# Optimization experiments

Measured on AMD Instinct MI355X. Metric: run time of the kernel, lower is better.

## Reference

```python
import jax, jax.numpy as jnp
import numpy as np
from jax import lax

NP = 27  # num_param, perfect cube
N3 = 3   # cube root
EPS = 1e-5


def _conv3d(x, w, stride, pad):
    return lax.conv_general_dilated(
        x, w, window_strides=(stride,) * 3, padding=[(pad, pad)] * 3,
        dimension_numbers=("NCDHW", "OIDHW", "NCDHW"))


def _p_n():
    # torch.meshgrid(arange(3),arange(3),arange(3), indexing='xy') == np.meshgrid 'xy'
    g0, g1, g2 = np.meshgrid(np.arange(N3), np.arange(N3), np.arange(N3), indexing="xy")
    p_n = np.concatenate([g0.ravel(), g1.ravel(), g2.ravel()], 0)  # (3N,)
    return jnp.asarray(p_n, jnp.float32).reshape(1, 3 * NP, 1, 1, 1)


def _p_0(h, w, d):
    # faithful to original: 'xy' meshgrid, flatten, then view(1,1,h,w,d)
    g0, g1, g2 = np.meshgrid(np.arange(h), np.arange(w), np.arange(d), indexing="xy")
    outs = []
    for g in (g0, g1, g2):
        gg = jnp.asarray(g.ravel(), jnp.float32).reshape(1, 1, h, w, d)
        outs.append(jnp.broadcast_to(gg, (1, NP, h, w, d)))
    return jnp.concatenate(outs, axis=1)  # (1, 3N, h, w, d)


def _gather_xq(x_flat, ix, iy, iz, W, D, shape):
    # x_flat: (b, c, H*W*D); i*: (b, h, w, d, N) int32
    idx = ix * (W * D) + iy * D + iz
    b = idx.shape[0]
    idx = jnp.clip(idx, 0, x_flat.shape[-1] - 1).reshape(b, -1)
    xq = jax.vmap(lambda xf, ii: xf[:, ii])(x_flat, idx)  # (b, c, h*w*d*N)
    return xq.reshape(shape)


def reference(x, p_w, p_b, conv_w, gamma, beta):
    b, c, H, W, D = x.shape
    # offset prediction (weight is zero-initialized in original; bias drives offsets)
    offset = _conv3d(x, p_w, 1, 1) + p_b[None, :, None, None, None]  # (b, 3N, h, w, d)
    h, w, d = offset.shape[2:]

    p = _p_0(h, w, d) + _p_n() + offset                 # (b, 3N, h, w, d)
    p = jnp.transpose(p, (0, 2, 3, 4, 1))               # (b, h, w, d, 3N)
    px, py, pz = p[..., :NP], p[..., NP:2 * NP], p[..., 2 * NP:]

    fx, fy, fz = jnp.floor(px), jnp.floor(py), jnp.floor(pz)
    ltx = jnp.clip(fx, 0, H - 1); lty = jnp.clip(fy, 0, W - 1); ltz = jnp.clip(fz, 0, D - 1)
    rbx = jnp.clip(fx + 1, 0, H - 1); rby = jnp.clip(fy + 1, 0, W - 1); rbz = jnp.clip(fz + 1, 0, D - 1)

    pcx = jnp.clip(px, 0, H - 1); pcy = jnp.clip(py, 0, W - 1); pcz = jnp.clip(pz, 0, D - 1)

    # trilinear-style weights (6 corners as in the original)
    g_lt = (1 + (ltx - pcx)) * (1 + (lty - pcy)) * (1 + (ltz - pcz))
    g_rb = (1 - (rbx - pcx)) * (1 - (rby - pcy)) * (1 - (rbz - pcz))
    g_lb = (1 + (ltx - pcx)) * (1 - (rby - pcy)) * (1 + (ltz - pcz))
    g_rt = (1 - (rbx - pcx)) * (1 + (lty - pcy)) * (1 + (ltz - pcz))
    g_lf = (1 + (ltx - pcx)) * (1 + (lty - pcy)) * (1 - (rbz - pcz))
    g_rf = (1 - (rbx - pcx)) * (1 - (rby - pcy)) * (1 + (ltz - pcz))

    i = lambda t: t.astype(jnp.int32)
    x_flat = x.reshape(b, c, -1)
    shp = (b, c, h, w, d, NP)
    xq_lt = _gather_xq(x_flat, i(ltx), i(lty), i(ltz), W, D, shp)
    xq_rb = _gather_xq(x_flat, i(rbx), i(rby), i(rbz), W, D, shp)
    xq_lb = _gather_xq(x_flat, i(ltx), i(rby), i(ltz), W, D, shp)
    xq_rt = _gather_xq(x_flat, i(rbx), i(lty), i(ltz), W, D, shp)
    xq_lf = _gather_xq(x_flat, i(ltx), i(lty), i(rbz), W, D, shp)
    xq_rf = _gather_xq(x_flat, i(rbx), i(rby), i(ltz), W, D, shp)

    e = lambda g: g[:, None]  # (b,1,h,w,d,N)
    x_off = (e(g_lt) * xq_lt + e(g_rb) * xq_rb + e(g_lb) * xq_lb +
             e(g_rt) * xq_rt + e(g_lf) * xq_lf + e(g_rf) * xq_rf)

    # regroup (b,c,h,w,d,27) -> (b,c,3h,3w,3d)
    x_off = x_off.reshape(b, c, h, w, d, N3, N3, N3)
    x_off = jnp.transpose(x_off, (0, 1, 2, 5, 3, 6, 4, 7)).reshape(b, c, h * N3, w * N3, d * N3)

    # Conv3d(stride 2, pad 1, no bias) + BatchNorm3d (train mode, batch stats) + SiLU
    o = _conv3d(x_off, conv_w, 2, 1)
    mean = jnp.mean(o, axis=(0, 2, 3, 4), keepdims=True)
    var = jnp.var(o, axis=(0, 2, 3, 4), keepdims=True)
    y = gamma[None, :, None, None, None] * (o - mean) * lax.rsqrt(var + EPS) + beta[None, :, None, None, None]
    return y * jax.nn.sigmoid(y)


def setup_inputs() -> dict:
    key = jax.random.key(0)
    k1, k2, k3 = jax.random.split(key, 3)
    B, Cin, Cout, S = 2, 16, 32, 32
    x = jax.random.normal(k1, (B, Cin, S, S, S), jnp.float32)
    p_w = jnp.zeros((3 * NP, Cin, 3, 3, 3), jnp.float32)  # zero-init as in original
    bound = 1.0 / np.sqrt(Cin * 27)
    p_b = jax.random.uniform(k2, (3 * NP,), jnp.float32, -bound, bound)
    conv_w = jax.random.normal(k3, (Cout, Cin, 3, 3, 3), jnp.float32) * 0.05
    gamma = jnp.ones((Cout,), jnp.float32)
    beta = jnp.zeros((Cout,), jnp.float32)
    return {"x": x, "p_w": p_w, "p_b": p_b, "conv_w": conv_w, "gamma": gamma, "beta": beta}
```

## Files before the change

kernel.cpp:

```cpp
#include <hip/hip_runtime.h>
#include <hip/hip_bf16.h>

constexpr int BATCH = 2;
constexpr int CIN   = 16;
constexpr int COUT  = 32;
constexpr int HWD   = 32768;
constexpr int OFFC  = 81;
constexpr int BIG   = 96;
constexpr int BIG2  = BIG * BIG;
constexpr int BIGN  = BIG * BIG * BIG;
constexpr int OUTD  = 48;
constexpr int OUT2  = OUTD * OUTD;
constexpr int OUTN  = OUTD * OUTD * OUTD;
constexpr int NOUT  = BATCH * COUT * OUTN;
constexpr int NBLK3 = 1728;

typedef __attribute__((ext_vector_type(8)))  short bf16x8;
typedef __attribute__((ext_vector_type(16))) float f32x16;

__device__ __forceinline__ float bf_lo(uint u) { return __uint_as_float(u << 16); }
__device__ __forceinline__ float bf_hi(uint u) { return __uint_as_float(u & 0xFFFF0000u); }

__global__ __launch_bounds__(256) void k_wtrans(const float* __restrict__ cw,
                                                const float* __restrict__ pw,
                                                ushort* __restrict__ wTb,
                                                ushort* __restrict__ pwTb) {
    int t = blockIdx.x * 256 + threadIdx.x;
    if (t < 13824) {
        int ci = t & 15; int rr = t >> 4; int co = rr & 31; int tap = rr >> 5;
        float v = cw[co * 432 + ci * 27 + tap];
        __hip_bfloat16 h = __float2bfloat16(v);
        wTb[t] = *(ushort*)&h;
    } else if (t < 13824 + 41472) {
        int u = t - 13824;
        int ci = u & 15; int rr = u >> 4; int oc = rr % 96; int tap = rr / 96;
        float v = (oc < 81) ? pw[oc * 432 + ci * 27 + tap] : 0.f;
        __hip_bfloat16 h = __float2bfloat16(v);
        pwTb[u] = *(ushort*)&h;
    }
}

__global__ __launch_bounds__(256) void k_xt(const float* __restrict__ x,
                                            ushort* __restrict__ xb) {
    int t = blockIdx.x * 256 + threadIdx.x;
    int bt = t >> 15, pos = t & 32767;
    float v[16];
#pragma unroll
    for (int ci = 0; ci < 16; ci++) v[ci] = x[(bt * 16 + ci) * HWD + pos];
    uint uw[8];
#pragma unroll
    for (int cc = 0; cc < 8; cc++) {
        __hip_bfloat16 h0 = __float2bfloat16(v[2 * cc]);
        __hip_bfloat16 h1 = __float2bfloat16(v[2 * cc + 1]);
        uw[cc] = (uint)(*(ushort*)&h0) | ((uint)(*(ushort*)&h1) << 16);
    }
    uint4* xd = (uint4*)(xb + (size_t)t * 16);
    xd[0] = make_uint4(uw[0], uw[1], uw[2], uw[3]);
    xd[1] = make_uint4(uw[4], uw[5], uw[6], uw[7]);
}

__global__ __launch_bounds__(256) void k_offset_mfma(const ushort* __restrict__ xb,
                                                     const ushort* __restrict__ pwTb,
                                                     const float* __restrict__ p_b,
                                                     float* __restrict__ off) {
    __shared__ uint4 lds[4 * 10 * 11 * 2];
    int blk = blockIdx.x;
    int bt = blk >> 8; int r = blk & 255;
    int ut = r >> 4; int vt = (r >> 2) & 3; int wt = r & 3;
    int a0 = ut * 2, b0 = vt * 8, c0 = wt * 8;
    int tid = threadIdx.x;
    int wv = tid >> 6, l = tid & 63, col = l & 31, half = l >> 5;

    const ushort* xbb = xb + (size_t)bt * HWD * 16;
    for (int s = tid; s < 800; s += 256) {
        int h = s & 1, p = s >> 1;
        int su = p / 100; int rm = p - su * 100;
        int sv = rm / 10; int sw = rm - sv * 10;
        int ga = a0 - 1 + su, gb = b0 - 1 + sv, gc = c0 - 1 + sw;
        uint4 v = make_uint4(0, 0, 0, 0);
        if ((unsigned)ga < 32u && (unsigned)gb < 32u && (unsigned)gc < 32u)
            v = *(const uint4*)(xbb + (size_t)(ga * 1024 + gb * 32 + gc) * 16 + h * 8);
        lds[((su * 10 + sv) * 11 + sw) * 2 + h] = v;
    }
    __syncthreads();

    int U = wv >> 1, V = ((wv & 1) << 2) + (col >> 3), W = col & 7;
    const uint4* wt4 = (const uint4*)pwTb;
    int a = a0 + U, b = b0 + V, c = c0 + W;
    int pos = a * 1024 + b * 32 + c;
    float* ob = off + (size_t)bt * OFFC * HWD + pos;

#pragma unroll 1
    for (int g = 0; g < 3; g++) {
        bf16x8 wf[27];
#pragma unroll
        for (int t = 0; t < 27; t++)
            wf[t] = __builtin_bit_cast(bf16x8, wt4[(t * 96 + g * 32 + col) * 2 + half]);
        f32x16 acc;
#pragma unroll
        for (int i = 0; i < 16; i++) acc[i] = 0.f;
#pragma unroll
        for (int k1 = 0; k1 < 3; k1++)
#pragma unroll
        for (int k2 = 0; k2 < 3; k2++)
#pragma unroll
        for (int k3 = 0; k3 < 3; k3++) {
            bf16x8 xf = __builtin_bit_cast(bf16x8,
                lds[(((U + k1) * 10 + (V + k2)) * 11 + (W + k3)) * 2 + half]);
            acc = __builtin_amdgcn_mfma_f32_32x32x16_bf16(wf[(k1 * 3 + k2) * 3 + k3],
                                                          xf, acc, 0, 0, 0);
        }
#pragma unroll
        for (int rg = 0; rg < 16; rg++) {
            int co = g * 32 + (rg & 3) + 8 * (rg >> 2) + 4 * half;
            if (co < 81) ob[(size_t)co * HWD] = acc[rg] + p_b[co];
        }
    }
}

__global__ __launch_bounds__(256, 3) void k_fused(const ushort* __restrict__ xb,
                                                  const float* __restrict__ off,
                                                  const ushort* __restrict__ wTb,
                                                  ushort* __restrict__ o16,
                                                  float* __restrict__ psum,
                                                  float* __restrict__ psq) {
    __shared__ uint4 lds[5 * 17 * 19 * 2];
    __shared__ float ls[4][32], lq[4][32];

    int blk = blockIdx.x;
    int bt = blk / 864; int r = blk - bt * 864;
    int ut = r / 36; r -= ut * 36;
    int vt = r / 6;  int wt = r - vt * 6;

    int tid = threadIdx.x;
    int wv = tid >> 6, l = tid & 63;
    int col = l & 31, half = l >> 5;

    const ushort* xbb = xb + (size_t)bt * HWD * 16;
    const float* offb = off + (size_t)bt * OFFC * HWD;
    int gU0 = ut * 4 - 1, gV0 = vt * 16 - 1, gW0 = wt * 16 - 1;

    for (int s = tid; s < 1445; s += 256) {
        int su = s / 289; int rm = s - su * 289;
        int sv = rm / 17; int sw = rm - sv * 17;
        int gU = gU0 + su, gV = gV0 + sv, gW = gW0 + sw;
        uint4 r0 = make_uint4(0, 0, 0, 0), r1 = r0;
        if ((unsigned)gU < 96u && (unsigned)gV < 96u && (unsigned)gW < 96u) {
            int a = gU / 3, i = gU - a * 3;
            int b = gV / 3, j = gV - b * 3;
            int c = gW / 3, kk = gW - c * 3;
            int n = i * 9 + j * 3 + kk;
            int pos = a * 1024 + b * 32 + c;
            float ox = offb[(size_t)n * HWD + pos];
            float oy = offb[(size_t)(27 + n) * HWD + pos];
            float oz = offb[(size_t)(54 + n) * HWD + pos];

            float px = (float)(b + j) + ox;
            float py = (float)(a + i) + oy;
            float pz = (float)(c + kk) + oz;

            float fx = floorf(px), fy = floorf(py), fz = floorf(pz);
            float ltx = fminf(fmaxf(fx, 0.f), 31.f);
            float lty = fminf(fmaxf(fy, 0.f), 31.f);
            float ltz = fminf(fmaxf(fz, 0.f), 31.f);
            float rbx = fminf(fmaxf(fx + 1.f, 0.f), 31.f);
            float rby = fminf(fmaxf(fy + 1.f, 0.f), 31.f);
            float rbz = fminf(fmaxf(fz + 1.f, 0.f), 31.f);
            float pcx = fminf(fmaxf(px, 0.f), 31.f);
            float pcy = fminf(fmaxf(py, 0.f), 31.f);
            float pcz = fminf(fmaxf(pz, 0.f), 31.f);

            float axl = 1.f + (ltx - pcx), axr = 1.f - (rbx - pcx);
            float ayl = 1.f + (lty - pcy), ayr = 1.f - (rby - pcy);
            float azl = 1.f + (ltz - pcz), azr = 1.f - (rbz - pcz);

            float g_lt = axl * ayl * azl;
            float g_rb = axr * ayr * azr;
            float g_lb = axl * ayr * azl;
            float g_rt = axr * ayl * azl;
            float g_lf = axl * ayl * azr;
            float g_rf = axr * ayr * azl;

            int iltx = (int)ltx, ilty = (int)lty, iltz = (int)ltz;
            int irbx = (int)rbx, irby = (int)rby, irbz = (int)rbz;

            int i_lt = iltx * 1024 + ilty * 32 + iltz;
            int i_rb = irbx * 1024 + irby * 32 + irbz;
            int i_lb = iltx * 1024 + irby * 32 + iltz;
            int i_rt = irbx * 1024 + ilty * 32 + iltz;
            int i_lf = iltx * 1024 + ilty * 32 + irbz;
            int i_rf = irbx * 1024 + irby * 32 + iltz;

            float acc[16];
#pragma unroll
            for (int q = 0; q < 16; q++) acc[q] = 0.f;

            auto corner = [&](float g, int ip) {
                const uint4* p = (const uint4*)(xbb + (size_t)ip * 16);
                uint4 u0 = p[0], u1 = p[1];
                acc[0]  += g * bf_lo(u0.x); acc[1]  += g * bf_hi(u0.x);
                acc[2]  += g * bf_lo(u0.y); acc[3]  += g * bf_hi(u0.y);
                acc[4]  += g * bf_lo(u0.z); acc[5]  += g * bf_hi(u0.z);
                acc[6]  += g * bf_lo(u0.w); acc[7]  += g * bf_hi(u0.w);
                acc[8]  += g * bf_lo(u1.x); acc[9]  += g * bf_hi(u1.x);
                acc[10] += g * bf_lo(u1.y); acc[11] += g * bf_hi(u1.y);
                acc[12] += g * bf_lo(u1.z); acc[13] += g * bf_hi(u1.z);
                acc[14] += g * bf_lo(u1.w); acc[15] += g * bf_hi(u1.w);
            };
            corner(g_lt, i_lt);
            corner(g_rb, i_rb);
            corner(g_lb, i_lb);
            corner(g_rt, i_rt);
            corner(g_lf, i_lf);
            corner(g_rf, i_rf);

            uint uw[8];
#pragma unroll
            for (int cc = 0; cc < 8; cc++) {
                __hip_bfloat16 h0 = __float2bfloat16(acc[2 * cc]);
                __hip_bfloat16 h1 = __float2bfloat16(acc[2 * cc + 1]);
                uw[cc] = (uint)(*(ushort*)&h0) | ((uint)(*(ushort*)&h1) << 16);
            }
            r0 = make_uint4(uw[0], uw[1], uw[2], uw[3]);
            r1 = make_uint4(uw[4], uw[5], uw[6], uw[7]);
        }
        int slot = (sw & 1) * 9 + (sw >> 1);
        lds[((su * 17 + sv) * 19 + slot) * 2 + 0] = r0;
        lds[((su * 17 + sv) * 19 + slot) * 2 + 1] = r1;
    }

    bf16x8 wf[27];
    const uint4* wt4 = (const uint4*)wTb;
#pragma unroll
    for (int t = 0; t < 27; t++)
        wf[t] = __builtin_bit_cast(bf16x8, wt4[(t * 32 + col) * 2 + half]);

    __syncthreads();

    int U = wv >> 1, V = (wv & 1) * 4 + (col >> 3), W = col & 7;
    const uint4* lp = &lds[(((2 * U * 17 + 2 * V) * 19) + W) * 2 + half];

    f32x16 acc;
#pragma unroll
    for (int i = 0; i < 16; i++) acc[i] = 0.f;

#pragma unroll
    for (int k1 = 0; k1 < 3; k1++)
#pragma unroll
    for (int k2 = 0; k2 < 3; k2++)
#pragma unroll
    for (int k3 = 0; k3 < 3; k3++) {
        const int so = (k3 == 0) ? 0 : (k3 == 1 ? 9 : 1);
        const int off2 = ((k1 * 17 + k2) * 19 + so) * 2;
        bf16x8 xf = __builtin_bit_cast(bf16x8, lp[off2]);
        acc = __builtin_amdgcn_mfma_f32_32x32x16_bf16(wf[(k1 * 3 + k2) * 3 + k3],
                                                      xf, acc, 0, 0, 0);
    }

    int u = ut * 2 + U, v = vt * 8 + V, wg = wt * 8 + W;
    size_t posg = (size_t)u * OUT2 + v * OUTD + wg;
    ushort* ob = o16 + (size_t)bt * COUT * OUTN;
#pragma unroll
    for (int rg = 0; rg < 16; rg++) {
        int co = (rg & 3) + 8 * (rg >> 2) + 4 * half;
        __hip_bfloat16 h = __float2bfloat16(acc[rg]);
        ob[(size_t)co * OUTN + posg] = *(ushort*)&h;
    }

#pragma unroll
    for (int rg = 0; rg < 16; rg++) {
        float s = acc[rg], q = acc[rg] * acc[rg];
#pragma unroll
        for (int o = 1; o < 32; o <<= 1) {
            s += __shfl_xor(s, o);
            q += __shfl_xor(q, o);
        }
        if (col == 0) {
            int co = (rg & 3) + 8 * (rg >> 2) + 4 * half;
            ls[wv][co] = s; lq[wv][co] = q;
        }
    }
    __syncthreads();
    if (tid < 32) {
        float s = ls[0][tid] + ls[1][tid] + ls[2][tid] + ls[3][tid];
        float q = lq[0][tid] + lq[1][tid] + lq[2][tid] + lq[3][tid];
        psum[blk * 32 + tid] = s;
        psq[blk * 32 + tid]  = q;
    }
}

__global__ __launch_bounds__(256) void k_stats(const float* __restrict__ psum,
                                               const float* __restrict__ psq,
                                               const float* __restrict__ gamma,
                                               const float* __restrict__ beta,
                                               float* __restrict__ stats) {
    int co  = blockIdx.x;
    int tid = threadIdx.x;
    float s = 0.f, q = 0.f;
    for (int i = tid; i < NBLK3; i += 256) {
        s += psum[i * 32 + co];
        q += psq[i * 32 + co];
    }
    __shared__ float ss[256], sq[256];
    ss[tid] = s; sq[tid] = q;
    __syncthreads();
    for (int st = 128; st > 0; st >>= 1) {
        if (tid < st) { ss[tid] += ss[tid + st]; sq[tid] += sq[tid + st]; }
        __syncthreads();
    }
    if (tid == 0) {
        const float N = 221184.f;
        float mean = ss[0] / N;
        float var  = sq[0] / N - mean * mean;
        float inv  = rsqrtf(var + 1e-5f);
        float A = gamma[co] * inv;
        stats[co * 2]     = A;
        stats[co * 2 + 1] = beta[co] - A * mean;
    }
}

__global__ __launch_bounds__(256) void k_bn_silu(const ushort* __restrict__ o16,
                                                 const float* __restrict__ stats,
                                                 float* __restrict__ out) {
    int t = blockIdx.x * 256 + threadIdx.x;
    int co = (t / (OUTN / 8)) & 31;
    float A = stats[co * 2], B = stats[co * 2 + 1];
    uint4 u = ((const uint4*)o16)[t];
    float o[8] = {bf_lo(u.x), bf_hi(u.x), bf_lo(u.y), bf_hi(u.y),
                  bf_lo(u.z), bf_hi(u.z), bf_lo(u.w), bf_hi(u.w)};
    float y[8];
#pragma unroll
    for (int q = 0; q < 8; q++) {
        float yy = A * o[q] + B;
        y[q] = yy / (1.f + __expf(-yy));
    }
    float4* dst = (float4*)(out + (size_t)t * 8);
    dst[0] = make_float4(y[0], y[1], y[2], y[3]);
    dst[1] = make_float4(y[4], y[5], y[6], y[7]);
}

extern "C" void kernel_launch(void* const* d_in, const int* in_sizes, int n_in,
                              void* d_out, int out_size, void* d_ws, size_t ws_size,
                              hipStream_t stream) {
    const float* x      = (const float*)d_in[0];
    const float* p_w    = (const float*)d_in[1];
    const float* p_b    = (const float*)d_in[2];
    const float* conv_w = (const float*)d_in[3];
    const float* gamma  = (const float*)d_in[4];
    const float* beta   = (const float*)d_in[5];
    float* out = (float*)d_out;
    float* ws  = (float*)d_ws;

    float* off   = ws;
    float* psum  = off + 5308416;
    float* psq   = psum + 55296;
    float* stats = psq + 55296;
    ushort* wTb  = (ushort*)(stats + 64);
    ushort* pwTb = wTb + 13824;
    ushort* xb   = pwTb + 41472;
    ushort* o16  = xb + 1048576;

    k_wtrans<<<216, 256, 0, stream>>>(conv_w, p_w, wTb, pwTb);
    k_xt<<<256, 256, 0, stream>>>(x, xb);
    k_offset_mfma<<<512, 256, 0, stream>>>(xb, pwTb, p_b, off);
    k_fused<<<NBLK3, 256, 0, stream>>>(xb, off, wTb, o16, psum, psq);
    k_stats<<<32, 256, 0, stream>>>(psum, psq, gamma, beta, stats);
    k_bn_silu<<<NOUT / 2048, 256, 0, stream>>>(o16, stats, out);
}
```

Before: 101.8 us.

## Store offsets as packed bf16 per position and remap fused block order

The offset conv now writes its results as bf16 in a position-major layout, with the x/y/z triple for each of the 27 sampling points packed into 4 ushorts. The fused kernel then fetches each triple with a single 8-byte load instead of three strided fp32 loads spread across channel planes. The fused kernel's block index is also permuted so that consecutive blocks map to different tiles and batches. The aim is to cut offset memory traffic and improve locality. In exchange, the offset stores become scattered 2-byte writes, and rounding the offsets to bf16 loses precision in the sampling coordinates.

```diff
diff --git a/kernel.cpp b/kernel.cpp
--- a/kernel.cpp
+++ b/kernel.cpp
@@ -62,7 +62,7 @@
 __global__ __launch_bounds__(256) void k_offset_mfma(const ushort* __restrict__ xb,
                                                      const ushort* __restrict__ pwTb,
                                                      const float* __restrict__ p_b,
-                                                     float* __restrict__ off) {
+                                                     ushort* __restrict__ offP) {
     __shared__ uint4 lds[4 * 10 * 11 * 2];
     int blk = blockIdx.x;
     int bt = blk >> 8; int r = blk & 255;
@@ -88,7 +88,7 @@
     const uint4* wt4 = (const uint4*)pwTb;
     int a = a0 + U, b = b0 + V, c = c0 + W;
     int pos = a * 1024 + b * 32 + c;
-    float* ob = off + (size_t)bt * OFFC * HWD + pos;
+    ushort* op = offP + ((size_t)bt * HWD + pos) * 108;
 
 #pragma unroll 1
     for (int g = 0; g < 3; g++) {
@@ -113,13 +113,17 @@
 #pragma unroll
         for (int rg = 0; rg < 16; rg++) {
             int co = g * 32 + (rg & 3) + 8 * (rg >> 2) + 4 * half;
-            if (co < 81) ob[(size_t)co * HWD] = acc[rg] + p_b[co];
+            if (co < 81) {
+                int n = co % 27, d = co / 27;
+                __hip_bfloat16 h = __float2bfloat16(acc[rg] + p_b[co]);
+                op[n * 4 + d] = *(ushort*)&h;
+            }
         }
     }
 }
 
 __global__ __launch_bounds__(256, 3) void k_fused(const ushort* __restrict__ xb,
-                                                  const float* __restrict__ off,
+                                                  const ushort* __restrict__ offP,
                                                   const ushort* __restrict__ wTb,
                                                   ushort* __restrict__ o16,
                                                   float* __restrict__ psum,
@@ -127,7 +131,8 @@
     __shared__ uint4 lds[5 * 17 * 19 * 2];
     __shared__ float ls[4][32], lq[4][32];
 
-    int blk = blockIdx.x;
+    int blk = (blockIdx.x & 7) * 216 + (blockIdx.x >> 3);
+
     int bt = blk / 864; int r = blk - bt * 864;
     int ut = r / 36; r -= ut * 36;
     int vt = r / 6;  int wt = r - vt * 6;
@@ -136,8 +141,8 @@
     int wv = tid >> 6, l = tid & 63;
     int col = l & 31, half = l >> 5;
 
-    const ushort* xbb = xb + (size_t)bt * HWD * 16;
-    const float* offb = off + (size_t)bt * OFFC * HWD;
+    const ushort* xbb  = xb + (size_t)bt * HWD * 16;
+    const ushort* offb = offP + (size_t)bt * HWD * 108;
     int gU0 = ut * 4 - 1, gV0 = vt * 16 - 1, gW0 = wt * 16 - 1;
 
     for (int s = tid; s < 1445; s += 256) {
@@ -151,9 +156,10 @@
             int c = gW / 3, kk = gW - c * 3;
             int n = i * 9 + j * 3 + kk;
             int pos = a * 1024 + b * 32 + c;
-            float ox = offb[(size_t)n * HWD + pos];
-            float oy = offb[(size_t)(27 + n) * HWD + pos];
-            float oz = offb[(size_t)(54 + n) * HWD + pos];
+            uint2 ou = *(const uint2*)(offb + (size_t)pos * 108 + n * 4);
+            float ox = bf_lo(ou.x);
+            float oy = bf_hi(ou.x);
+            float oz = bf_lo(ou.y);
 
             float px = (float)(b + j) + ox;
             float py = (float)(a + i) + oy;
@@ -351,19 +357,19 @@
     float* out = (float*)d_out;
     float* ws  = (float*)d_ws;
 
-    float* off   = ws;
-    float* psum  = off + 5308416;
+    float* psum  = ws;
     float* psq   = psum + 55296;
     float* stats = psq + 55296;
     ushort* wTb  = (ushort*)(stats + 64);
     ushort* pwTb = wTb + 13824;
     ushort* xb   = pwTb + 41472;
-    ushort* o16  = xb + 1048576;
+    ushort* offP = xb + 1048576;
+    ushort* o16  = offP + 7077888;
 
     k_wtrans<<<216, 256, 0, stream>>>(conv_w, p_w, wTb, pwTb);
     k_xt<<<256, 256, 0, stream>>>(x, xb);
-    k_offset_mfma<<<512, 256, 0, stream>>>(xb, pwTb, p_b, off);
-    k_fused<<<NBLK3, 256, 0, stream>>>(xb, off, wTb, o16, psum, psq);
+    k_offset_mfma<<<512, 256, 0, stream>>>(xb, pwTb, p_b, offP);
+    k_fused<<<NBLK3, 256, 0, stream>>>(xb, offP, wTb, o16, psum, psq);
     k_stats<<<32, 256, 0, stream>>>(psum, psq, gamma, beta, stats);
     k_bn_silu<<<NOUT / 2048, 256, 0, stream>>>(o16, stats, out);
 }
```

Result: no change. 102.0 us (+0.2%).
